# Kernel tuning notes

Hardware: AMD Instinct MI355X
Metric: run time of the kernel (lower is better)

The kernel has to match this reference:

```python
import jax, jax.numpy as jnp
import numpy as np

B, N, F_, H, K_IN, K = 2, 768, 128, 128, 2, 2
TAU = 0.66


def setup_inputs() -> dict:
    key = jax.random.key(0)
    ks = jax.random.split(key, 8)
    s = lambda fan: 1.0 / np.sqrt(fan)
    X = jax.random.normal(ks[0], (B, N, F_), jnp.float32)
    # edge_feat RezeroMLP: Linear(F,H) -> act -> Linear(H,H)
    ef_w1 = jax.random.normal(ks[1], (F_, H), jnp.float32) * s(F_)
    ef_b1 = jnp.zeros((H,), jnp.float32)
    ef_w2 = jax.random.normal(ks[2], (H, H), jnp.float32) * s(H)
    ef_b2 = jnp.zeros((H,), jnp.float32)
    # rezero gate (init 0 in module; use small nonzero so the branch is exercised)
    gate = jnp.asarray(0.1, jnp.float32)
    # score_mlp RezeroMLP: Linear(k_in,H) -> ReLU -> Linear(H,k)
    sm_w1 = jax.random.normal(ks[3], (K_IN, H), jnp.float32) * s(K_IN)
    sm_b1 = jnp.zeros((H,), jnp.float32)
    sm_w2 = jax.random.normal(ks[4], (H, K), jnp.float32) * s(H)
    sm_b2 = jnp.zeros((K,), jnp.float32)
    # pre-sampled standard Gumbel noise for gumbel_softmax
    u = jax.random.uniform(ks[5], (B, N, N, K), jnp.float32, minval=1e-6, maxval=1.0 - 1e-6)
    gumbel = -jnp.log(-jnp.log(u))
    return {"X": X, "ef_w1": ef_w1, "ef_b1": ef_b1, "ef_w2": ef_w2, "ef_b2": ef_b2,
            "gate": gate, "sm_w1": sm_w1, "sm_b1": sm_b1, "sm_w2": sm_w2, "sm_b2": sm_b2,
            "gumbel": gumbel}


def reference(X, ef_w1, ef_b1, ef_w2, ef_b2, gate, sm_w1, sm_b1, sm_w2, sm_b2, gumbel):
    # edge_feat MLP: [B,N,F] -> [B,N,H]
    feats = jax.nn.relu(X @ ef_w1 + ef_b1) @ ef_w2 + ef_b2
    D = H // K_IN
    Xact = feats.reshape(B, N, D, K_IN)
    Xskip = X.reshape(B, N, D, K_IN)  # feat_dim == hidden_dim, proj is None
    Xc = (Xskip + gate * Xact).transpose(0, 3, 1, 2)  # [B,k_in,N,D]
    # pairwise outer product ('prod' scoring): [B,N,N,k_in]
    prod = jnp.einsum('bkid,bkjd->bijk', Xc, Xc)
    # per-edge score MLP: k_in -> H -> k
    scores = jax.nn.relu(prod @ sm_w1 + sm_b1) @ sm_w2 + sm_b2  # [B,N,N,k]
    logits = scores - jnp.max(scores, axis=-1, keepdims=True)
    # gumbel-softmax, hard (straight-through)
    y_soft = jax.nn.softmax((logits + gumbel) / TAU, axis=-1)
    y_hard = jax.nn.one_hot(jnp.argmax(y_soft, axis=-1), K, dtype=y_soft.dtype)
    y = y_hard + y_soft - jax.lax.stop_gradient(y_soft)
    # A = y @ zo with zo = [0,1,...]: probability/one-hot mass of 'edge' states
    zo = jnp.ones((K,), y.dtype).at[0].set(0.0)
    A = y @ zo  # [B,N,N]
    # zero diagonal and symmetrize via upper triangle
    Au = jnp.triu(A, 1)
    return Au + jnp.swapaxes(Au, -1, -2)
```

## Files before the change

### kernel.cpp

```cpp
#include <hip/hip_runtime.h>

#define BB 2
#define NN 768
#define FF 128
#define HH 128
#define TS 32
#define NT (NN / TS)
#define NPAIR (NT * (NT + 1) / 2)
#define EROWS 2
#define THR 4e-3f

__device__ __forceinline__
double edge_exact_f64(const double* __restrict__ Xc, const double* __restrict__ wpack,
                      int b, int i, int j, double init) {
    const double* xi0 = Xc + ((size_t)(b * 2 + 0) * NN + i) * 64;
    const double* xj0 = Xc + ((size_t)(b * 2 + 0) * NN + j) * 64;
    const double* xi1 = Xc + ((size_t)(b * 2 + 1) * NN + i) * 64;
    const double* xj1 = Xc + ((size_t)(b * 2 + 1) * NN + j) * 64;
    double p0 = 0.0, p1 = 0.0;
#pragma unroll 4
    for (int d2 = 0; d2 < 32; ++d2) {
        double2 a0 = *(const double2*)&xi0[2 * d2];
        double2 b0 = *(const double2*)&xj0[2 * d2];
        double2 a1 = *(const double2*)&xi1[2 * d2];
        double2 b1 = *(const double2*)&xj1[2 * d2];
        p0 = fma(a0.y, b0.y, fma(a0.x, b0.x, p0));
        p1 = fma(a1.y, b1.y, fma(a1.x, b1.x, p1));
    }
    double m = init;
#pragma unroll 8
    for (int c = 0; c < HH; ++c) {
        double2 wab = *(const double2*)&wpack[4 * c];
        double2 wbw = *(const double2*)&wpack[4 * c + 2];
        double tt = fma(p1, wab.y, fma(p0, wab.x, wbw.x));
        tt = fmax(tt, 0.0);
        m = fma(tt, wbw.y, m);
    }
    return m;
}

__global__ __launch_bounds__(128)
void edgefeat_kernel(const float* __restrict__ X,
                     const float* __restrict__ w1, const float* __restrict__ b1,
                     const float* __restrict__ w2, const float* __restrict__ b2,
                     const float* __restrict__ gatep,
                     const float* __restrict__ sm_w1, const float* __restrict__ sm_b1,
                     const float* __restrict__ sm_w2,
                     double* __restrict__ Xc, float* __restrict__ Xcf,
                     double* __restrict__ wpack, float4* __restrict__ wpackf) {
    __shared__ float  Xs[EROWS][FF];
    __shared__ double Hs[EROWS][HH];
    const int h = threadIdx.x;
    const int row0 = blockIdx.x * EROWS;
    for (int r = 0; r < EROWS; ++r) Xs[r][h] = X[(size_t)(row0 + r) * FF + h];
    if (blockIdx.x == 0) {
        double a  = (double)sm_w1[h];
        double bq = (double)sm_w1[HH + h];
        double be = (double)sm_b1[h];
        double wd = (double)sm_w2[2 * h + 1] - (double)sm_w2[2 * h + 0];
        wpack[4 * h + 0] = a;  wpack[4 * h + 1] = bq;
        wpack[4 * h + 2] = be; wpack[4 * h + 3] = wd;
        wpackf[h] = make_float4((float)a, (float)bq, (float)be, (float)wd);
    }
    __syncthreads();
    double acc[EROWS];
    double bb = (double)b1[h];
    for (int r = 0; r < EROWS; ++r) acc[r] = bb;
    for (int f = 0; f < FF; ++f) {
        double w = (double)w1[f * HH + h];
        for (int r = 0; r < EROWS; ++r) acc[r] = fma((double)Xs[r][f], w, acc[r]);
    }
    for (int r = 0; r < EROWS; ++r) Hs[r][h] = acc[r] > 0.0 ? acc[r] : 0.0;
    __syncthreads();
    bb = (double)b2[h];
    for (int r = 0; r < EROWS; ++r) acc[r] = bb;
    for (int c = 0; c < HH; ++c) {
        double w = (double)w2[c * HH + h];
        for (int r = 0; r < EROWS; ++r) acc[r] = fma(Hs[r][c], w, acc[r]);
    }
    const double gate = (double)gatep[0];
    const int k = h & 1, d = h >> 1;
    const int b = row0 / NN;
    const int i0 = row0 % NN;
    for (int r = 0; r < EROWS; ++r) {
        double v = (double)Xs[r][h] + gate * acc[r];
        size_t idx = (((size_t)(b * 2 + k)) * NN + (i0 + r)) * 64 + d;
        Xc[idx]  = v;
        Xcf[idx] = (float)v;
    }
}

__global__ __launch_bounds__(512, 6)
void edge_decide_kernel(const double* __restrict__ Xc,
                        const float* __restrict__ Xcf,
                        const double* __restrict__ wpack,
                        const float4* __restrict__ wpackf,
                        const float* __restrict__ sm_b2,
                        const float* __restrict__ gumbel,
                        float* __restrict__ out) {
    __shared__ float  Ai[2][TS][66];
    __shared__ float  Aj[2][TS][66];
    __shared__ float4 Wl[HH];
    __shared__ float  As[TS][TS + 1];
    const int b = blockIdx.y;
    const int t = blockIdx.x;
    int ti = (int)((49.0 - sqrt(2401.0 - 8.0 * (double)t)) * 0.5);
    int base = ti * (49 - ti) / 2;
    if (t < base) { --ti; base = ti * (49 - ti) / 2; }
    else { int nb = (ti + 1) * (48 - ti) / 2; if (t >= nb) { ++ti; base = nb; } }
    const int tj = t - base + ti;
    const int tid = threadIdx.x;
    const int i0 = ti * TS, j0 = tj * TS;

    for (int q = 0; q < 4; ++q) {
        int flat = tid + 512 * q;
        int dp = flat & 31;
        int r  = (flat >> 5) & 31;
        int k  = flat >> 10;
        size_t rowbase = ((size_t)(b * 2 + k)) * NN;
        *(float2*)&Ai[k][r][2 * dp] = *(const float2*)&Xcf[(rowbase + i0 + r) * 64 + 2 * dp];
        *(float2*)&Aj[k][r][2 * dp] = *(const float2*)&Xcf[(rowbase + j0 + r) * 64 + 2 * dp];
    }
    if (tid < HH) Wl[tid] = wpackf[tid];

    const int s  = tid & 1;
    const int e  = tid >> 1;
    const int rh = e >> 4;
    const int ch = e & 15;
    const int r0 = rh, r1 = rh + 16;
    const int c0 = 2 * ch, c1 = c0 + 1;
    const int gi0 = i0 + r0, gi1 = i0 + r1;
    const int gj0 = j0 + c0, gj1 = j0 + c1;

    float4 g0v = make_float4(0.f, 0.f, 0.f, 0.f);
    float4 g1v = make_float4(0.f, 0.f, 0.f, 0.f);
    if (s == 0) {
        g0v = *(const float4*)&gumbel[(((size_t)b * NN + gi0) * NN + gj0) * 2];
        g1v = *(const float4*)&gumbel[(((size_t)b * NN + gi1) * NN + gj0) * 2];
    }
    __syncthreads();

    float p000 = 0.f, p001 = 0.f, p010 = 0.f, p011 = 0.f;
    float p100 = 0.f, p101 = 0.f, p110 = 0.f, p111 = 0.f;
#pragma unroll
    for (int it = 0; it < 16; ++it) {
        const int d2 = s + 2 * it;
        float2 a00 = *(const float2*)&Ai[0][r0][2 * d2];
        float2 a01 = *(const float2*)&Ai[0][r1][2 * d2];
        float2 a10 = *(const float2*)&Ai[1][r0][2 * d2];
        float2 a11 = *(const float2*)&Ai[1][r1][2 * d2];
        float2 b00 = *(const float2*)&Aj[0][c0][2 * d2];
        float2 b01 = *(const float2*)&Aj[0][c1][2 * d2];
        float2 b10 = *(const float2*)&Aj[1][c0][2 * d2];
        float2 b11 = *(const float2*)&Aj[1][c1][2 * d2];
        p000 = fmaf(a00.y, b00.y, fmaf(a00.x, b00.x, p000));
        p001 = fmaf(a00.y, b01.y, fmaf(a00.x, b01.x, p001));
        p010 = fmaf(a01.y, b00.y, fmaf(a01.x, b00.x, p010));
        p011 = fmaf(a01.y, b01.y, fmaf(a01.x, b01.x, p011));
        p100 = fmaf(a10.y, b10.y, fmaf(a10.x, b10.x, p100));
        p101 = fmaf(a10.y, b11.y, fmaf(a10.x, b11.x, p101));
        p110 = fmaf(a11.y, b10.y, fmaf(a11.x, b10.x, p110));
        p111 = fmaf(a11.y, b11.y, fmaf(a11.x, b11.x, p111));
    }
    p000 += __shfl_xor(p000, 1); p001 += __shfl_xor(p001, 1);
    p010 += __shfl_xor(p010, 1); p011 += __shfl_xor(p011, 1);
    p100 += __shfl_xor(p100, 1); p101 += __shfl_xor(p101, 1);
    p110 += __shfl_xor(p110, 1); p111 += __shfl_xor(p111, 1);

    float m00 = 0.f, m01 = 0.f, m10 = 0.f, m11 = 0.f;
#pragma unroll 8
    for (int it = 0; it < 64; ++it) {
        float4 w = Wl[s + 2 * it];
        float tt;
        tt = fmaf(p100, w.y, fmaf(p000, w.x, w.z)); tt = fmaxf(tt, 0.f); m00 = fmaf(tt, w.w, m00);
        tt = fmaf(p101, w.y, fmaf(p001, w.x, w.z)); tt = fmaxf(tt, 0.f); m01 = fmaf(tt, w.w, m01);
        tt = fmaf(p110, w.y, fmaf(p010, w.x, w.z)); tt = fmaxf(tt, 0.f); m10 = fmaf(tt, w.w, m10);
        tt = fmaf(p111, w.y, fmaf(p011, w.x, w.z)); tt = fmaxf(tt, 0.f); m11 = fmaf(tt, w.w, m11);
    }
    m00 += __shfl_xor(m00, 1); m01 += __shfl_xor(m01, 1);
    m10 += __shfl_xor(m10, 1); m11 += __shfl_xor(m11, 1);

    if (s == 0) {
        const double bd = (double)sm_b2[1] - (double)sm_b2[0];
        double i00 = bd + ((double)g0v.y - (double)g0v.x);
        double i01 = bd + ((double)g0v.w - (double)g0v.z);
        double i10 = bd + ((double)g1v.y - (double)g1v.x);
        double i11 = bd + ((double)g1v.w - (double)g1v.z);
        float f00 = m00 + (float)i00;
        float f01 = m01 + (float)i01;
        float f10 = m10 + (float)i10;
        float f11 = m11 + (float)i11;
        float A00 = f00 > 0.f ? 1.f : 0.f;
        float A01 = f01 > 0.f ? 1.f : 0.f;
        float A10 = f10 > 0.f ? 1.f : 0.f;
        float A11 = f11 > 0.f ? 1.f : 0.f;
        float fm = fminf(fminf(fabsf(f00), fabsf(f01)), fminf(fabsf(f10), fabsf(f11)));
        if (__builtin_expect(fm < THR, 0)) {
            if (fabsf(f00) < THR) A00 = edge_exact_f64(Xc, wpack, b, gi0, gj0, i00) > 0.0 ? 1.f : 0.f;
            if (fabsf(f01) < THR) A01 = edge_exact_f64(Xc, wpack, b, gi0, gj1, i01) > 0.0 ? 1.f : 0.f;
            if (fabsf(f10) < THR) A10 = edge_exact_f64(Xc, wpack, b, gi1, gj0, i10) > 0.0 ? 1.f : 0.f;
            if (fabsf(f11) < THR) A11 = edge_exact_f64(Xc, wpack, b, gi1, gj1, i11) > 0.0 ? 1.f : 0.f;
        }
        As[r0][c0] = A00; As[r0][c1] = A01;
        As[r1][c0] = A10; As[r1][c1] = A11;
    }
    __syncthreads();

    if (s == 0) {
        float A00 = As[r0][c0], A01 = As[r0][c1];
        float A10 = As[r1][c0], A11 = As[r1][c1];
        if (ti != tj) {
            *(float2*)&out[((size_t)b * NN + gi0) * NN + gj0] = make_float2(A00, A01);
            *(float2*)&out[((size_t)b * NN + gi1) * NN + gj0] = make_float2(A10, A11);
            float2 t0 = make_float2(As[c0][r0], As[c1][r0]);
            *(float2*)&out[((size_t)b * NN + j0 + r0) * NN + i0 + c0] = t0;
            float2 t1 = make_float2(As[c0][r1], As[c1][r1]);
            *(float2*)&out[((size_t)b * NN + j0 + r1) * NN + i0 + c0] = t1;
        } else {
            float v00 = (r0 < c0) ? A00 : ((r0 > c0) ? As[c0][r0] : 0.0f);
            float v01 = (r0 < c1) ? A01 : ((r0 > c1) ? As[c1][r0] : 0.0f);
            float v10 = (r1 < c0) ? A10 : ((r1 > c0) ? As[c0][r1] : 0.0f);
            float v11 = (r1 < c1) ? A11 : ((r1 > c1) ? As[c1][r1] : 0.0f);
            *(float2*)&out[((size_t)b * NN + gi0) * NN + gj0] = make_float2(v00, v01);
            *(float2*)&out[((size_t)b * NN + gi1) * NN + gj0] = make_float2(v10, v11);
        }
    }
}

extern "C" void kernel_launch(void* const* d_in, const int* in_sizes, int n_in,
                              void* d_out, int out_size, void* d_ws, size_t ws_size,
                              hipStream_t stream) {
    const float* X      = (const float*)d_in[0];
    const float* ef_w1  = (const float*)d_in[1];
    const float* ef_b1  = (const float*)d_in[2];
    const float* ef_w2  = (const float*)d_in[3];
    const float* ef_b2  = (const float*)d_in[4];
    const float* gate   = (const float*)d_in[5];
    const float* sm_w1  = (const float*)d_in[6];
    const float* sm_b1  = (const float*)d_in[7];
    const float* sm_w2  = (const float*)d_in[8];
    const float* sm_b2  = (const float*)d_in[9];
    const float* gumbel = (const float*)d_in[10];
    float* out = (float*)d_out;

    double* Xc     = (double*)d_ws;
    double* wpack  = Xc + (size_t)BB * 2 * NN * 64;
    float4* wpackf = (float4*)(wpack + 4 * HH);
    float*  Xcf    = (float*)(wpackf + HH);

    edgefeat_kernel<<<BB * NN / EROWS, 128, 0, stream>>>(
        X, ef_w1, ef_b1, ef_w2, ef_b2, gate, sm_w1, sm_b1, sm_w2, Xc, Xcf, wpack, wpackf);
    dim3 grid(NPAIR, BB);
    edge_decide_kernel<<<grid, 512, 0, stream>>>(Xc, Xcf, wpack, wpackf, sm_b2, gumbel, out);
}
```

Measured before the change: 120.5 us.

## Replace per-edge score MLP with angular piecewise-linear lookup when bias is zero

When sm_b1 is all zero, the ReLU MLP over the 2-d input is positively homogeneous, so its output is linear within angular sectors bounded by the hidden units' zero lines. The first kernel now sorts these 256 breakpoint angles, builds a bin index, and precomputes per-sector linear coefficients. Each edge then evaluates one atan2, a short search and one FMA instead of 128 hidden units. The original loop remains as a fallback for nonzero bias, and the existing fp64 recheck near the threshold still guards borderline decisions. The table build runs serially in block 0 of the feature kernel, and the gumbel load now happens on both lanes.

```diff
diff --git a/kernel.cpp b/kernel.cpp
--- a/kernel.cpp
+++ b/kernel.cpp
@@ -9,6 +9,10 @@
 #define NPAIR (NT * (NT + 1) / 2)
 #define EROWS 2
 #define THR 4e-3f
+
+#define PIf   3.14159265358979323846f
+#define PI2f  1.57079632679489661923f
+#define TPIf  6.28318530717958647692f
 
 __device__ __forceinline__
 double edge_exact_f64(const double* __restrict__ Xc, const double* __restrict__ wpack,
@@ -47,13 +51,20 @@
                      const float* __restrict__ sm_w1, const float* __restrict__ sm_b1,
                      const float* __restrict__ sm_w2,
                      double* __restrict__ Xc, float* __restrict__ Xcf,
-                     double* __restrict__ wpack, float4* __restrict__ wpackf) {
+                     double* __restrict__ wpack, float4* __restrict__ wpackf,
+                     float2* __restrict__ ABg, float* __restrict__ bpg,
+                     unsigned* __restrict__ bsg, unsigned* __restrict__ flg) {
     __shared__ float  Xs[EROWS][FF];
     __shared__ double Hs[EROWS][HH];
+    __shared__ float  sbp[256];
+    __shared__ float  sWa[128], sWb[128], sWw[128];
+    __shared__ int    snz;
     const int h = threadIdx.x;
     const int row0 = blockIdx.x * EROWS;
     for (int r = 0; r < EROWS; ++r) Xs[r][h] = X[(size_t)(row0 + r) * FF + h];
+
     if (blockIdx.x == 0) {
+        if (h == 0) snz = 0;
         double a  = (double)sm_w1[h];
         double bq = (double)sm_w1[HH + h];
         double be = (double)sm_b1[h];
@@ -61,8 +72,48 @@
         wpack[4 * h + 0] = a;  wpack[4 * h + 1] = bq;
         wpack[4 * h + 2] = be; wpack[4 * h + 3] = wd;
         wpackf[h] = make_float4((float)a, (float)bq, (float)be, (float)wd);
+        sWa[h] = (float)a; sWb[h] = (float)bq; sWw[h] = (float)wd;
+        __syncthreads();
+        if (be != 0.0) atomicOr(&snz, 1);
+        float phi = (float)atan2(bq, a);
+        float t1 = phi + PI2f; if (t1 >= PIf) t1 -= TPIf;
+        float t2 = phi - PI2f; if (t2 < -PIf) t2 += TPIf;
+        sbp[h] = t1; sbp[h + 128] = t2;
+        for (int k = 2; k <= 256; k <<= 1) {
+            for (int j = k >> 1; j > 0; j >>= 1) {
+                __syncthreads();
+                int i  = ((h & ~(j - 1)) << 1) | (h & (j - 1));
+                int ix = i | j;
+                float x = sbp[i], y = sbp[ix];
+                bool up = ((i & k) == 0);
+                if ((x > y) == up) { sbp[i] = y; sbp[ix] = x; }
+            }
+        }
+        __syncthreads();
+        bpg[h] = sbp[h]; bpg[h + 128] = sbp[h + 128];
+        for (int bin = h; bin <= 256; bin += 128) {
+            float left = -PIf + (float)bin * (PIf / 128.0f);
+            int cnt = 0;
+            for (int i2 = 0; i2 < 256; ++i2) cnt += (sbp[i2] < left) ? 1 : 0;
+            bsg[bin] = (unsigned)cnt;
+        }
+        for (int sec = h; sec < 256; sec += 128) {
+            float lo = sbp[sec];
+            float hi = (sec < 255) ? sbp[sec + 1] : sbp[0] + TPIf;
+            float thm = 0.5f * (lo + hi), sn, cs;
+            __sincosf(thm, &sn, &cs);
+            float A = 0.f, B = 0.f;
+            for (int c2 = 0; c2 < 128; ++c2) {
+                float hv = fmaf(sWa[c2], cs, sWb[c2] * sn);
+                if (hv > 0.f) { A = fmaf(sWw[c2], sWa[c2], A); B = fmaf(sWw[c2], sWb[c2], B); }
+            }
+            ABg[sec] = make_float2(A, B);
+        }
+        __syncthreads();
+        if (h == 0) flg[0] = (unsigned)snz;
     }
     __syncthreads();
+
     double acc[EROWS];
     double bb = (double)b1[h];
     for (int r = 0; r < EROWS; ++r) acc[r] = bb;
@@ -90,18 +141,36 @@
     }
 }
 
+__device__ __forceinline__
+float lut_eval(float p0, float p1, const float* __restrict__ bpl,
+               const unsigned* __restrict__ bsl, const float2* __restrict__ ABl) {
+    float th = atan2f(p1, p0);
+    int bin = (int)((th + PIf) * (128.0f / PIf));
+    bin = bin < 0 ? 0 : (bin > 255 ? 255 : bin);
+    int idx = (int)bsl[bin];
+    while (idx < 256 && bpl[idx] <= th) ++idx;
+    int sec = (idx == 0) ? 255 : idx - 1;
+    float2 ab = ABl[sec];
+    return fmaf(ab.x, p0, ab.y * p1);
+}
+
 __global__ __launch_bounds__(512, 6)
 void edge_decide_kernel(const double* __restrict__ Xc,
                         const float* __restrict__ Xcf,
                         const double* __restrict__ wpack,
                         const float4* __restrict__ wpackf,
+                        const float2* __restrict__ ABg, const float* __restrict__ bpg,
+                        const unsigned* __restrict__ bsg, const unsigned* __restrict__ flg,
                         const float* __restrict__ sm_b2,
                         const float* __restrict__ gumbel,
                         float* __restrict__ out) {
     __shared__ float  Ai[2][TS][66];
     __shared__ float  Aj[2][TS][66];
+    __shared__ float  As[TS][TS + 1];
     __shared__ float4 Wl[HH];
-    __shared__ float  As[TS][TS + 1];
+    __shared__ float  bpl[256];
+    __shared__ float2 ABl[256];
+    __shared__ unsigned bsl[256];
     const int b = blockIdx.y;
     const int t = blockIdx.x;
     int ti = (int)((49.0 - sqrt(2401.0 - 8.0 * (double)t)) * 0.5);
@@ -121,7 +190,9 @@
         *(float2*)&Ai[k][r][2 * dp] = *(const float2*)&Xcf[(rowbase + i0 + r) * 64 + 2 * dp];
         *(float2*)&Aj[k][r][2 * dp] = *(const float2*)&Xcf[(rowbase + j0 + r) * 64 + 2 * dp];
     }
-    if (tid < HH) Wl[tid] = wpackf[tid];
+    if (tid < 256) { bpl[tid] = bpg[tid]; ABl[tid] = ABg[tid]; bsl[tid] = bsg[tid]; }
+    if (tid < HH)  Wl[tid] = wpackf[tid];
+    const unsigned biased = flg[0];
 
     const int s  = tid & 1;
     const int e  = tid >> 1;
@@ -132,12 +203,8 @@
     const int gi0 = i0 + r0, gi1 = i0 + r1;
     const int gj0 = j0 + c0, gj1 = j0 + c1;
 
-    float4 g0v = make_float4(0.f, 0.f, 0.f, 0.f);
-    float4 g1v = make_float4(0.f, 0.f, 0.f, 0.f);
-    if (s == 0) {
-        g0v = *(const float4*)&gumbel[(((size_t)b * NN + gi0) * NN + gj0) * 2];
-        g1v = *(const float4*)&gumbel[(((size_t)b * NN + gi1) * NN + gj0) * 2];
-    }
+    float4 g0v = *(const float4*)&gumbel[(((size_t)b * NN + gi0) * NN + gj0) * 2];
+    float4 g1v = *(const float4*)&gumbel[(((size_t)b * NN + gi1) * NN + gj0) * 2];
     __syncthreads();
 
     float p000 = 0.f, p001 = 0.f, p010 = 0.f, p011 = 0.f;
@@ -167,39 +234,48 @@
     p100 += __shfl_xor(p100, 1); p101 += __shfl_xor(p101, 1);
     p110 += __shfl_xor(p110, 1); p111 += __shfl_xor(p111, 1);
 
-    float m00 = 0.f, m01 = 0.f, m10 = 0.f, m11 = 0.f;
+    const double bd = (double)sm_b2[1] - (double)sm_b2[0];
+    double i00 = bd + ((double)g0v.y - (double)g0v.x);
+    double i01 = bd + ((double)g0v.w - (double)g0v.z);
+    double i10 = bd + ((double)g1v.y - (double)g1v.x);
+    double i11 = bd + ((double)g1v.w - (double)g1v.z);
+
+    float m00, m01, m10, m11;
+    if (!biased) {
+        float pa0 = (s == 0) ? p000 : p010, pa1 = (s == 0) ? p100 : p110;
+        float pb0 = (s == 0) ? p001 : p011, pb1 = (s == 0) ? p101 : p111;
+        float ia  = (s == 0) ? (float)i00 : (float)i10;
+        float ib  = (s == 0) ? (float)i01 : (float)i11;
+        float ma = lut_eval(pa0, pa1, bpl, bsl, ABl) + ia;
+        float mb = lut_eval(pb0, pb1, bpl, bsl, ABl) + ib;
+        float moa = __shfl_xor(ma, 1);
+        float mob = __shfl_xor(mb, 1);
+        m00 = (s == 0) ? ma : moa;  m01 = (s == 0) ? mb : mob;
+        m10 = (s == 0) ? moa : ma;  m11 = (s == 0) ? mob : mb;
+    } else {
+        m00 = (float)i00; m01 = (float)i01; m10 = (float)i10; m11 = (float)i11;
 #pragma unroll 8
-    for (int it = 0; it < 64; ++it) {
-        float4 w = Wl[s + 2 * it];
-        float tt;
-        tt = fmaf(p100, w.y, fmaf(p000, w.x, w.z)); tt = fmaxf(tt, 0.f); m00 = fmaf(tt, w.w, m00);
-        tt = fmaf(p101, w.y, fmaf(p001, w.x, w.z)); tt = fmaxf(tt, 0.f); m01 = fmaf(tt, w.w, m01);
-        tt = fmaf(p110, w.y, fmaf(p010, w.x, w.z)); tt = fmaxf(tt, 0.f); m10 = fmaf(tt, w.w, m10);
-        tt = fmaf(p111, w.y, fmaf(p011, w.x, w.z)); tt = fmaxf(tt, 0.f); m11 = fmaf(tt, w.w, m11);
-    }
-    m00 += __shfl_xor(m00, 1); m01 += __shfl_xor(m01, 1);
-    m10 += __shfl_xor(m10, 1); m11 += __shfl_xor(m11, 1);
+        for (int c = 0; c < HH; ++c) {
+            float4 w = Wl[c];
+            float tt;
+            tt = fmaf(p100, w.y, fmaf(p000, w.x, w.z)); tt = fmaxf(tt, 0.f); m00 = fmaf(tt, w.w, m00);
+            tt = fmaf(p101, w.y, fmaf(p001, w.x, w.z)); tt = fmaxf(tt, 0.f); m01 = fmaf(tt, w.w, m01);
+            tt = fmaf(p110, w.y, fmaf(p010, w.x, w.z)); tt = fmaxf(tt, 0.f); m10 = fmaf(tt, w.w, m10);
+            tt = fmaf(p111, w.y, fmaf(p011, w.x, w.z)); tt = fmaxf(tt, 0.f); m11 = fmaf(tt, w.w, m11);
+        }
+    }
 
     if (s == 0) {
-        const double bd = (double)sm_b2[1] - (double)sm_b2[0];
-        double i00 = bd + ((double)g0v.y - (double)g0v.x);
-        double i01 = bd + ((double)g0v.w - (double)g0v.z);
-        double i10 = bd + ((double)g1v.y - (double)g1v.x);
-        double i11 = bd + ((double)g1v.w - (double)g1v.z);
-        float f00 = m00 + (float)i00;
-        float f01 = m01 + (float)i01;
-        float f10 = m10 + (float)i10;
-        float f11 = m11 + (float)i11;
-        float A00 = f00 > 0.f ? 1.f : 0.f;
-        float A01 = f01 > 0.f ? 1.f : 0.f;
-        float A10 = f10 > 0.f ? 1.f : 0.f;
-        float A11 = f11 > 0.f ? 1.f : 0.f;
-        float fm = fminf(fminf(fabsf(f00), fabsf(f01)), fminf(fabsf(f10), fabsf(f11)));
+        float A00 = m00 > 0.f ? 1.f : 0.f;
+        float A01 = m01 > 0.f ? 1.f : 0.f;
+        float A10 = m10 > 0.f ? 1.f : 0.f;
+        float A11 = m11 > 0.f ? 1.f : 0.f;
+        float fm = fminf(fminf(fabsf(m00), fabsf(m01)), fminf(fabsf(m10), fabsf(m11)));
         if (__builtin_expect(fm < THR, 0)) {
-            if (fabsf(f00) < THR) A00 = edge_exact_f64(Xc, wpack, b, gi0, gj0, i00) > 0.0 ? 1.f : 0.f;
-            if (fabsf(f01) < THR) A01 = edge_exact_f64(Xc, wpack, b, gi0, gj1, i01) > 0.0 ? 1.f : 0.f;
-            if (fabsf(f10) < THR) A10 = edge_exact_f64(Xc, wpack, b, gi1, gj0, i10) > 0.0 ? 1.f : 0.f;
-            if (fabsf(f11) < THR) A11 = edge_exact_f64(Xc, wpack, b, gi1, gj1, i11) > 0.0 ? 1.f : 0.f;
+            if (fabsf(m00) < THR) A00 = edge_exact_f64(Xc, wpack, b, gi0, gj0, i00) > 0.0 ? 1.f : 0.f;
+            if (fabsf(m01) < THR) A01 = edge_exact_f64(Xc, wpack, b, gi0, gj1, i01) > 0.0 ? 1.f : 0.f;
+            if (fabsf(m10) < THR) A10 = edge_exact_f64(Xc, wpack, b, gi1, gj0, i10) > 0.0 ? 1.f : 0.f;
+            if (fabsf(m11) < THR) A11 = edge_exact_f64(Xc, wpack, b, gi1, gj1, i11) > 0.0 ? 1.f : 0.f;
         }
         As[r0][c0] = A00; As[r0][c1] = A01;
         As[r1][c0] = A10; As[r1][c1] = A11;
@@ -243,13 +319,19 @@
     const float* gumbel = (const float*)d_in[10];
     float* out = (float*)d_out;
 
-    double* Xc     = (double*)d_ws;
-    double* wpack  = Xc + (size_t)BB * 2 * NN * 64;
-    float4* wpackf = (float4*)(wpack + 4 * HH);
-    float*  Xcf    = (float*)(wpackf + HH);
+    double*   Xc     = (double*)d_ws;
+    double*   wpack  = Xc + (size_t)BB * 2 * NN * 64;
+    float4*   wpackf = (float4*)(wpack + 4 * HH);
+    float2*   ABg    = (float2*)(wpackf + HH);
+    float*    bpg    = (float*)(ABg + 256);
+    unsigned* bsg    = (unsigned*)(bpg + 256);
+    unsigned* flg    = bsg + 260;
+    float*    Xcf    = (float*)(flg + 4);
 
     edgefeat_kernel<<<BB * NN / EROWS, 128, 0, stream>>>(
-        X, ef_w1, ef_b1, ef_w2, ef_b2, gate, sm_w1, sm_b1, sm_w2, Xc, Xcf, wpack, wpackf);
+        X, ef_w1, ef_b1, ef_w2, ef_b2, gate, sm_w1, sm_b1, sm_w2,
+        Xc, Xcf, wpack, wpackf, ABg, bpg, bsg, flg);
     dim3 grid(NPAIR, BB);
-    edge_decide_kernel<<<grid, 512, 0, stream>>>(Xc, Xcf, wpack, wpackf, sm_b2, gumbel, out);
-}
+    edge_decide_kernel<<<grid, 512, 0, stream>>>(
+        Xc, Xcf, wpack, wpackf, ABg, bpg, bsg, flg, sm_b2, gumbel, out);
+}
```

Measured after the change: 146.1 us. 1.21x slower.
